# Kernel optimization log

Measured on AMD Instinct MI355X. Metric: run time of the kernel, lower is better.

Reference implementation:

```python
import jax, jax.numpy as jnp
import numpy as np

EPS = 1e-6

def rmsnorm(x):
    # RMSNormalize: x / sqrt(mean(x^2) + eps) over last dim (no learnable scale)
    return x * jax.lax.rsqrt(jnp.mean(jnp.square(x), axis=-1, keepdims=True) + EPS)

def setup_inputs() -> dict:
    key = jax.random.key(0)
    ks = jax.random.split(key, 7)
    B, S, D, H = 8, 4096, 1024, 128
    x = jax.random.normal(ks[0], (B, S, D), dtype=jnp.float32)
    # nn.Linear init scale ~ 1/sqrt(fan_in)
    W0 = jax.random.normal(ks[1], (D, H), dtype=jnp.float32) / np.sqrt(D)
    b0 = jax.random.normal(ks[2], (H,), dtype=jnp.float32) / np.sqrt(D)
    W1 = jax.random.normal(ks[3], (H, H), dtype=jnp.float32) / np.sqrt(H)
    b1 = jax.random.normal(ks[4], (H,), dtype=jnp.float32) / np.sqrt(H)
    W2 = jax.random.normal(ks[5], (H, H), dtype=jnp.float32) / np.sqrt(H)
    b2 = jax.random.normal(ks[6], (H,), dtype=jnp.float32) / np.sqrt(H)
    return {"x": x, "W0": W0, "b0": b0, "W1": W1, "b1": b1, "W2": W2, "b2": b2}

def reference(x, W0, b0, W1, b1, W2, b2):
    h = jnp.einsum('bsd,dh->bsh', x, W0) + b0          # linear(in_features -> 128)
    h = rmsnorm(h)                                      # RMSNormalize
    h = jax.nn.sigmoid(jnp.einsum('bsh,hk->bsk', h, W1) + b1) + h  # sigmoid block + residual
    h = jax.nn.relu(jnp.einsum('bsh,hk->bsk', h, W2) + b2) + h     # relu block + residual
    return h
```

## Files before the change

kernel.cpp:

```cpp
#include <hip/hip_runtime.h>
#include <hip/hip_bf16.h>


using u16    = unsigned short;
using f32x4  = __attribute__((ext_vector_type(4))) float;
using bf16x8 = __attribute__((ext_vector_type(8))) short;
using u16x8  = __attribute__((ext_vector_type(8))) unsigned short;

__device__ __forceinline__ float bf2f(u16 u) {
  union { unsigned int i; float f; } v; v.i = ((unsigned int)u) << 16; return v.f;
}
__device__ __forceinline__ u16 f2bf(float f) {
  union { float f; unsigned int i; } v; v.f = f;
  unsigned int r = v.i + 0x7fffu + ((v.i >> 16) & 1u);
  return (u16)(r >> 16);
}

#define WS_W0T 64
#define WS_W1T 262208
#define WS_W2T 294976
#define WS_BIAS 327744

__device__ __forceinline__ int hoff(int row, int col) {
  return row * 256 + (((col >> 3) ^ (row & 7)) << 4) + ((col & 7) << 1);
}

__global__ void __launch_bounds__(256)
prep_kernel(const float* __restrict__ W0, const float* __restrict__ W1,
            const float* __restrict__ W2, const float* __restrict__ b0,
            const float* __restrict__ b1, const float* __restrict__ b2,
            char* __restrict__ wsb) {
  const int bid = blockIdx.x;
  if (bid == 160) {
    float* bias = (float*)(wsb + WS_BIAS);
    for (int i = threadIdx.x; i < 384; i += 256) {
      int which = i >> 7, j = i & 127;
      const float* src = (which == 0) ? b0 : (which == 1) ? b1 : b2;
      bias[i] = src[j];
    }
    return;
  }
  __shared__ float tile[32][33];
  const float* src; u16* dst; int K, N, kt, nt;
  if (bid < 128)      { src = W0; dst = (u16*)(wsb + WS_W0T); K = 1024; N = 128; kt = bid >> 2;         nt = bid & 3; }
  else if (bid < 144) { src = W1; dst = (u16*)(wsb + WS_W1T); K = 128;  N = 128; kt = (bid - 128) >> 2; nt = (bid - 128) & 3; }
  else                { src = W2; dst = (u16*)(wsb + WS_W2T); K = 128;  N = 128; kt = (bid - 144) >> 2; nt = (bid - 144) & 3; }
  const int tx = threadIdx.x & 31, ty = threadIdx.x >> 5;
#pragma unroll
  for (int i = 0; i < 4; ++i) {
    int k = kt * 32 + ty + i * 8, n = nt * 32 + tx;
    tile[ty + i * 8][tx] = src[(size_t)k * N + n];
  }
  __syncthreads();
#pragma unroll
  for (int i = 0; i < 4; ++i) {
    int n = nt * 32 + ty + i * 8, k = kt * 32 + tx;
    dst[(size_t)n * K + k] = f2bf(tile[tx][ty + i * 8]);
  }
}

__global__ void __launch_bounds__(512)
fused_kernel(const float* __restrict__ xin, const char* __restrict__ wsb,
             float* __restrict__ outv) {
  __shared__ char smem[65536];
  char* xs  = smem;
  char* wsm = smem + 16384;
  char* hns = smem;
  char* h1s = smem + 32768;

  const u16* w0t    = (const u16*)(wsb + WS_W0T);
  const u16* w1t    = (const u16*)(wsb + WS_W1T);
  const u16* w2t    = (const u16*)(wsb + WS_W2T);
  const float* bias = (const float*)(wsb + WS_BIAS);

  const int tid    = threadIdx.x;
  const int lane   = tid & 63;
  const int wave   = tid >> 6;
  const int lane16 = lane & 15;
  const int quad   = lane >> 4;
  const int m_base = (wave & 3) * 32;
  const int n_base = (wave >> 2) * 64;
  const int row0   = blockIdx.x * 128;

  float b0v[4], b1v[4], b2v[4];
#pragma unroll
  for (int nt = 0; nt < 4; ++nt) {
    int col = n_base + nt * 16 + lane16;
    b0v[nt] = bias[col]; b1v[nt] = bias[128 + col]; b2v[nt] = bias[256 + col];
  }

  const int r0 = tid >> 3, c0 = tid & 7, r1 = r0 + 64;

  u16x8 sx[2], sw[2];
  auto preload = [&](int k0) {
#pragma unroll
    for (int i = 0; i < 2; ++i) {
      int r = (i == 0) ? r0 : r1;
      size_t eoff = (size_t)(row0 + r) * 1024 + k0 + c0 * 8;
      const float* p = xin + eoff;
      f32x4 f0 = *(const f32x4*)p;
      f32x4 f1 = *(const f32x4*)(p + 4);
      u16x8 t;
#pragma unroll
      for (int e = 0; e < 4; ++e) { t[e] = f2bf(f0[e]); t[e + 4] = f2bf(f1[e]); }
      sx[i] = t;
      sw[i] = *(const u16x8*)(w0t + (size_t)r * 1024 + k0 + c0 * 8);
    }
  };

  f32x4 acc[2][4] = {};
  preload(0);

  for (int s = 0; s < 16; ++s) {
    __syncthreads();
#pragma unroll
    for (int i = 0; i < 2; ++i) {
      int r = (i == 0) ? r0 : r1;
      int p = c0 ^ (r & 7);
      *(u16x8*)(xs  + r * 128 + p * 16) = sx[i];
      *(u16x8*)(wsm + r * 128 + p * 16) = sw[i];
    }
    __syncthreads();
    if (s < 15) preload((s + 1) * 64);
#pragma unroll
    for (int kk = 0; kk < 2; ++kk) {
      int ph = ((kk * 4 + quad) ^ (lane & 7)) << 4;
      bf16x8 a[2], b[4];
#pragma unroll
      for (int rh = 0; rh < 2; ++rh)
        a[rh] = *(const bf16x8*)(xs + (m_base + rh * 16 + lane16) * 128 + ph);
#pragma unroll
      for (int nt = 0; nt < 4; ++nt)
        b[nt] = *(const bf16x8*)(wsm + (n_base + nt * 16 + lane16) * 128 + ph);
#pragma unroll
      for (int rh = 0; rh < 2; ++rh)
#pragma unroll
        for (int nt = 0; nt < 4; ++nt)
          acc[rh][nt] = __builtin_amdgcn_mfma_f32_16x16x32_bf16(
              a[rh], b[nt], acc[rh][nt], 0, 0, 0);
    }
  }
  __syncthreads();

#pragma unroll
  for (int rh = 0; rh < 2; ++rh)
#pragma unroll
    for (int nt = 0; nt < 4; ++nt) {
      int col = n_base + nt * 16 + lane16;
#pragma unroll
      for (int r = 0; r < 4; ++r) {
        int row = m_base + rh * 16 + quad * 4 + r;
        *(u16*)(hns + hoff(row, col)) = f2bf(acc[rh][nt][r] + b0v[nt]);
      }
    }
  __syncthreads();

  {
    int r = tid >> 2, qq = tid & 3;
    u16x8 vals[4];
    float ss = 0.f;
#pragma unroll
    for (int j = 0; j < 4; ++j) {
      int c = qq * 4 + j;
      vals[j] = *(const u16x8*)(hns + r * 256 + ((c ^ (r & 7)) << 4));
#pragma unroll
      for (int e = 0; e < 8; ++e) { float f = bf2f(vals[j][e]); ss += f * f; }
    }
    ss += __shfl_xor(ss, 1);
    ss += __shfl_xor(ss, 2);
    float scale = rsqrtf(ss * (1.f / 128.f) + 1e-6f);
#pragma unroll
    for (int j = 0; j < 4; ++j) {
      u16x8 o;
#pragma unroll
      for (int e = 0; e < 8; ++e) o[e] = f2bf(bf2f(vals[j][e]) * scale);
      int c = qq * 4 + j;
      *(u16x8*)(hns + r * 256 + ((c ^ (r & 7)) << 4)) = o;
    }
  }
  __syncthreads();

  f32x4 acc1[2][4] = {};
#pragma unroll
  for (int kk = 0; kk < 4; ++kk) {
    int ph = ((kk * 4 + quad) ^ (lane & 7)) << 4;
    bf16x8 a[2], b[4];
#pragma unroll
    for (int rh = 0; rh < 2; ++rh)
      a[rh] = *(const bf16x8*)(hns + (m_base + rh * 16 + lane16) * 256 + ph);
#pragma unroll
    for (int nt = 0; nt < 4; ++nt)
      b[nt] = *(const bf16x8*)(w1t + (size_t)(n_base + nt * 16 + lane16) * 128 +
                               kk * 32 + quad * 8);
#pragma unroll
    for (int rh = 0; rh < 2; ++rh)
#pragma unroll
      for (int nt = 0; nt < 4; ++nt)
        acc1[rh][nt] = __builtin_amdgcn_mfma_f32_16x16x32_bf16(
            a[rh], b[nt], acc1[rh][nt], 0, 0, 0);
  }
#pragma unroll
  for (int rh = 0; rh < 2; ++rh)
#pragma unroll
    for (int nt = 0; nt < 4; ++nt) {
      int col = n_base + nt * 16 + lane16;
#pragma unroll
      for (int r = 0; r < 4; ++r) {
        int row = m_base + rh * 16 + quad * 4 + r;
        int o = hoff(row, col);
        float hn = bf2f(*(const u16*)(hns + o));
        float v = acc1[rh][nt][r] + b1v[nt];
        *(u16*)(h1s + o) = f2bf(hn + 1.f / (1.f + __expf(-v)));
      }
    }
  __syncthreads();

  f32x4 acc2[2][4] = {};
#pragma unroll
  for (int kk = 0; kk < 4; ++kk) {
    int ph = ((kk * 4 + quad) ^ (lane & 7)) << 4;
    bf16x8 a[2], b[4];
#pragma unroll
    for (int rh = 0; rh < 2; ++rh)
      a[rh] = *(const bf16x8*)(h1s + (m_base + rh * 16 + lane16) * 256 + ph);
#pragma unroll
    for (int nt = 0; nt < 4; ++nt)
      b[nt] = *(const bf16x8*)(w2t + (size_t)(n_base + nt * 16 + lane16) * 128 +
                               kk * 32 + quad * 8);
#pragma unroll
    for (int rh = 0; rh < 2; ++rh)
#pragma unroll
      for (int nt = 0; nt < 4; ++nt)
        acc2[rh][nt] = __builtin_amdgcn_mfma_f32_16x16x32_bf16(
            a[rh], b[nt], acc2[rh][nt], 0, 0, 0);
  }
#pragma unroll
  for (int rh = 0; rh < 2; ++rh)
#pragma unroll
    for (int nt = 0; nt < 4; ++nt) {
      int col = n_base + nt * 16 + lane16;
#pragma unroll
      for (int r = 0; r < 4; ++r) {
        int row = m_base + rh * 16 + quad * 4 + r;
        float h1v = bf2f(*(const u16*)(h1s + hoff(row, col)));
        float v = acc2[rh][nt][r] + b2v[nt];
        float res = h1v + fmaxf(v, 0.f);
        outv[(size_t)(row0 + row) * 128 + col] = res;
      }
    }
}

extern "C" void kernel_launch(void* const* d_in, const int* in_sizes, int n_in,
                              void* d_out, int out_size, void* d_ws, size_t ws_size,
                              hipStream_t stream) {
  const float* x  = (const float*)d_in[0];
  const float* W0 = (const float*)d_in[1];
  const float* b0 = (const float*)d_in[2];
  const float* W1 = (const float*)d_in[3];
  const float* b1 = (const float*)d_in[4];
  const float* W2 = (const float*)d_in[5];
  const float* b2 = (const float*)d_in[6];
  char* wsb = (char*)d_ws;

  prep_kernel<<<161, 256, 0, stream>>>(W0, W1, W2, b0, b1, b2, wsb);
  fused_kernel<<<256, 512, 0, stream>>>(x, wsb, (float*)d_out);
}
```

Baseline: 226.9 us.

## Halve row tile, double-buffer the LDS K-loop, and launch more blocks

The row tile per block drops from 128 to 64 rows. Each of the 8 waves now computes a 32x32 output tile, and the grid doubles to 512 blocks so each CU gets two blocks instead of one. The first GEMM's K-loop now uses two LDS buffers holding raw fp32 x prefetched into registers, which cuts synchronisation to one barrier per stage and overlaps global loads with MFMA work. The goal is to hide memory latency in a kernel that looks latency-bound. The cost is that W0 is re-read from cache twice as often across blocks, and the bf16 conversion now happens at staging time.

```diff
diff --git a/kernel.cpp b/kernel.cpp
--- a/kernel.cpp
+++ b/kernel.cpp
@@ -59,14 +59,12 @@
   }
 }
 
-__global__ void __launch_bounds__(512)
+__global__ void __launch_bounds__(512, 4)
 fused_kernel(const float* __restrict__ xin, const char* __restrict__ wsb,
              float* __restrict__ outv) {
-  __shared__ char smem[65536];
-  char* xs  = smem;
-  char* wsm = smem + 16384;
+  __shared__ char smem[49152];
   char* hns = smem;
-  char* h1s = smem + 32768;
+  char* h1s = smem + 16384;
 
   const u16* w0t    = (const u16*)(wsb + WS_W0T);
   const u16* w1t    = (const u16*)(wsb + WS_W1T);
@@ -78,74 +76,82 @@
   const int wave   = tid >> 6;
   const int lane16 = lane & 15;
   const int quad   = lane >> 4;
-  const int m_base = (wave & 3) * 32;
-  const int n_base = (wave >> 2) * 64;
-  const int row0   = blockIdx.x * 128;
-
-  float b0v[4], b1v[4], b2v[4];
-#pragma unroll
-  for (int nt = 0; nt < 4; ++nt) {
-    int col = n_base + nt * 16 + lane16;
-    b0v[nt] = bias[col]; b1v[nt] = bias[128 + col]; b2v[nt] = bias[256 + col];
-  }
-
-  const int r0 = tid >> 3, c0 = tid & 7, r1 = r0 + 64;
-
-  u16x8 sx[2], sw[2];
-  auto preload = [&](int k0) {
-#pragma unroll
-    for (int i = 0; i < 2; ++i) {
-      int r = (i == 0) ? r0 : r1;
-      size_t eoff = (size_t)(row0 + r) * 1024 + k0 + c0 * 8;
-      const float* p = xin + eoff;
-      f32x4 f0 = *(const f32x4*)p;
-      f32x4 f1 = *(const f32x4*)(p + 4);
-      u16x8 t;
-#pragma unroll
-      for (int e = 0; e < 4; ++e) { t[e] = f2bf(f0[e]); t[e + 4] = f2bf(f1[e]); }
-      sx[i] = t;
-      sw[i] = *(const u16x8*)(w0t + (size_t)r * 1024 + k0 + c0 * 8);
-    }
+  const int m_base = (wave & 1) * 32;
+  const int n_base = (wave >> 1) * 32;
+  const int row0   = blockIdx.x * 64;
+
+  const int rx  = tid >> 3;
+  const int cx  = tid & 7;
+  const int xsw = (cx ^ (rx & 7)) << 4;
+
+  f32x4 xA0, xA1, xB0, xB1;
+  u16x8 wA0, wA1, wB0, wB1;
+
+  auto preload = [&](f32x4& x0, f32x4& x1, u16x8& w0, u16x8& w1, int k0) {
+    const float* p = xin + (size_t)(row0 + rx) * 1024 + k0 + cx * 8;
+    x0 = *(const f32x4*)p;
+    x1 = *(const f32x4*)(p + 4);
+    const u16* wp = w0t + (size_t)rx * 1024 + k0 + cx * 8;
+    w0 = *(const u16x8*)wp;
+    w1 = *(const u16x8*)(wp + 65536);
   };
 
-  f32x4 acc[2][4] = {};
-  preload(0);
-
-  for (int s = 0; s < 16; ++s) {
-    __syncthreads();
-#pragma unroll
-    for (int i = 0; i < 2; ++i) {
-      int r = (i == 0) ? r0 : r1;
-      int p = c0 ^ (r & 7);
-      *(u16x8*)(xs  + r * 128 + p * 16) = sx[i];
-      *(u16x8*)(wsm + r * 128 + p * 16) = sw[i];
-    }
-    __syncthreads();
-    if (s < 15) preload((s + 1) * 64);
+  auto stage = [&](char* xs, char* wsm, const f32x4& x0, const f32x4& x1,
+                   const u16x8& w0, const u16x8& w1) {
+    u16x8 t;
+#pragma unroll
+    for (int e = 0; e < 4; ++e) { t[e] = f2bf(x0[e]); t[e + 4] = f2bf(x1[e]); }
+    *(u16x8*)(xs + rx * 128 + xsw) = t;
+    *(u16x8*)(wsm + rx * 128 + xsw) = w0;
+    *(u16x8*)(wsm + (rx + 64) * 128 + xsw) = w1;
+  };
+
+  f32x4 acc[2][2] = {};
+
+  auto mmac = [&](const char* xs, const char* wsm) {
 #pragma unroll
     for (int kk = 0; kk < 2; ++kk) {
       int ph = ((kk * 4 + quad) ^ (lane & 7)) << 4;
-      bf16x8 a[2], b[4];
+      bf16x8 a[2], b[2];
 #pragma unroll
       for (int rh = 0; rh < 2; ++rh)
         a[rh] = *(const bf16x8*)(xs + (m_base + rh * 16 + lane16) * 128 + ph);
 #pragma unroll
-      for (int nt = 0; nt < 4; ++nt)
+      for (int nt = 0; nt < 2; ++nt)
         b[nt] = *(const bf16x8*)(wsm + (n_base + nt * 16 + lane16) * 128 + ph);
 #pragma unroll
       for (int rh = 0; rh < 2; ++rh)
 #pragma unroll
-        for (int nt = 0; nt < 4; ++nt)
+        for (int nt = 0; nt < 2; ++nt)
           acc[rh][nt] = __builtin_amdgcn_mfma_f32_16x16x32_bf16(
               a[rh], b[nt], acc[rh][nt], 0, 0, 0);
     }
-  }
-  __syncthreads();
+  };
+
+  float b0v[2];
+#pragma unroll
+  for (int nt = 0; nt < 2; ++nt) b0v[nt] = bias[n_base + nt * 16 + lane16];
+
+  preload(xA0, xA1, wA0, wA1, 0);
+  preload(xB0, xB1, wB0, wB1, 64);
+
+  for (int ss = 0; ss < 8; ++ss) {
+    const int s0 = ss * 2;
+    stage(smem, smem + 8192, xA0, xA1, wA0, wA1);
+    if (s0 + 2 < 16) preload(xA0, xA1, wA0, wA1, (s0 + 2) * 64);
+    __syncthreads();
+    mmac(smem, smem + 8192);
+
+    stage(smem + 24576, smem + 32768, xB0, xB1, wB0, wB1);
+    if (s0 + 3 < 16) preload(xB0, xB1, wB0, wB1, (s0 + 3) * 64);
+    __syncthreads();
+    mmac(smem + 24576, smem + 32768);
+  }
 
 #pragma unroll
   for (int rh = 0; rh < 2; ++rh)
 #pragma unroll
-    for (int nt = 0; nt < 4; ++nt) {
+    for (int nt = 0; nt < 2; ++nt) {
       int col = n_base + nt * 16 + lane16;
 #pragma unroll
       for (int r = 0; r < 4; ++r) {
@@ -156,53 +162,57 @@
   __syncthreads();
 
   {
-    int r = tid >> 2, qq = tid & 3;
-    u16x8 vals[4];
-    float ss = 0.f;
-#pragma unroll
-    for (int j = 0; j < 4; ++j) {
-      int c = qq * 4 + j;
+    int r = tid >> 3, q = tid & 7;
+    u16x8 vals[2];
+    float sum = 0.f;
+#pragma unroll
+    for (int j = 0; j < 2; ++j) {
+      int c = q * 2 + j;
       vals[j] = *(const u16x8*)(hns + r * 256 + ((c ^ (r & 7)) << 4));
 #pragma unroll
-      for (int e = 0; e < 8; ++e) { float f = bf2f(vals[j][e]); ss += f * f; }
-    }
-    ss += __shfl_xor(ss, 1);
-    ss += __shfl_xor(ss, 2);
-    float scale = rsqrtf(ss * (1.f / 128.f) + 1e-6f);
-#pragma unroll
-    for (int j = 0; j < 4; ++j) {
+      for (int e = 0; e < 8; ++e) { float f = bf2f(vals[j][e]); sum += f * f; }
+    }
+    sum += __shfl_xor(sum, 1);
+    sum += __shfl_xor(sum, 2);
+    sum += __shfl_xor(sum, 4);
+    float scale = rsqrtf(sum * (1.f / 128.f) + 1e-6f);
+#pragma unroll
+    for (int j = 0; j < 2; ++j) {
       u16x8 o;
 #pragma unroll
       for (int e = 0; e < 8; ++e) o[e] = f2bf(bf2f(vals[j][e]) * scale);
-      int c = qq * 4 + j;
+      int c = q * 2 + j;
       *(u16x8*)(hns + r * 256 + ((c ^ (r & 7)) << 4)) = o;
     }
   }
   __syncthreads();
 
-  f32x4 acc1[2][4] = {};
+  float b1v[2];
+#pragma unroll
+  for (int nt = 0; nt < 2; ++nt) b1v[nt] = bias[128 + n_base + nt * 16 + lane16];
+  f32x4 acc1[2][2] = {};
 #pragma unroll
   for (int kk = 0; kk < 4; ++kk) {
     int ph = ((kk * 4 + quad) ^ (lane & 7)) << 4;
-    bf16x8 a[2], b[4];
+    bf16x8 a[2], b[2];
 #pragma unroll
     for (int rh = 0; rh < 2; ++rh)
       a[rh] = *(const bf16x8*)(hns + (m_base + rh * 16 + lane16) * 256 + ph);
 #pragma unroll
-    for (int nt = 0; nt < 4; ++nt)
+    for (int nt = 0; nt < 2; ++nt)
       b[nt] = *(const bf16x8*)(w1t + (size_t)(n_base + nt * 16 + lane16) * 128 +
                                kk * 32 + quad * 8);
 #pragma unroll
     for (int rh = 0; rh < 2; ++rh)
 #pragma unroll
-      for (int nt = 0; nt < 4; ++nt)
+      for (int nt = 0; nt < 2; ++nt)
         acc1[rh][nt] = __builtin_amdgcn_mfma_f32_16x16x32_bf16(
             a[rh], b[nt], acc1[rh][nt], 0, 0, 0);
   }
 #pragma unroll
   for (int rh = 0; rh < 2; ++rh)
 #pragma unroll
-    for (int nt = 0; nt < 4; ++nt) {
+    for (int nt = 0; nt < 2; ++nt) {
       int col = n_base + nt * 16 + lane16;
 #pragma unroll
       for (int r = 0; r < 4; ++r) {
@@ -215,29 +225,32 @@
     }
   __syncthreads();
 
-  f32x4 acc2[2][4] = {};
+  float b2v[2];
+#pragma unroll
+  for (int nt = 0; nt < 2; ++nt) b2v[nt] = bias[256 + n_base + nt * 16 + lane16];
+  f32x4 acc2[2][2] = {};
 #pragma unroll
   for (int kk = 0; kk < 4; ++kk) {
     int ph = ((kk * 4 + quad) ^ (lane & 7)) << 4;
-    bf16x8 a[2], b[4];
+    bf16x8 a[2], b[2];
 #pragma unroll
     for (int rh = 0; rh < 2; ++rh)
       a[rh] = *(const bf16x8*)(h1s + (m_base + rh * 16 + lane16) * 256 + ph);
 #pragma unroll
-    for (int nt = 0; nt < 4; ++nt)
+    for (int nt = 0; nt < 2; ++nt)
       b[nt] = *(const bf16x8*)(w2t + (size_t)(n_base + nt * 16 + lane16) * 128 +
                                kk * 32 + quad * 8);
 #pragma unroll
     for (int rh = 0; rh < 2; ++rh)
 #pragma unroll
-      for (int nt = 0; nt < 4; ++nt)
+      for (int nt = 0; nt < 2; ++nt)
         acc2[rh][nt] = __builtin_amdgcn_mfma_f32_16x16x32_bf16(
             a[rh], b[nt], acc2[rh][nt], 0, 0, 0);
   }
 #pragma unroll
   for (int rh = 0; rh < 2; ++rh)
 #pragma unroll
-    for (int nt = 0; nt < 4; ++nt) {
+    for (int nt = 0; nt < 2; ++nt) {
       int col = n_base + nt * 16 + lane16;
 #pragma unroll
       for (int r = 0; r < 4; ++r) {
@@ -263,5 +276,5 @@
   char* wsb = (char*)d_ws;
 
   prep_kernel<<<161, 256, 0, stream>>>(W0, W1, W2, b0, b1, b2, wsb);
-  fused_kernel<<<256, 512, 0, stream>>>(x, wsb, (float*)d_out);
-}
+  fused_kernel<<<512, 512, 0, stream>>>(x, wsb, (float*)d_out);
+}
```

Result: faster. 219.4 us (-3.3%).
